# Performance work log

Measured on AMD Instinct MI355X. Metric: run time of the kernel, lower is better.

The kernel has to match this reference:

```python
import jax, jax.numpy as jnp
import numpy as np

N_NODES = 100000


def gcn_conv(x, W, b, src, dst, num_nodes):
    """PyG GCNConv: out = D^{-1/2} (A + I) D^{-1/2} (x W) + b, messages src->dst."""
    h = x @ W  # [N, out]
    # degree with self-loops (edge weight 1)
    deg = jax.ops.segment_sum(jnp.ones(src.shape[0], dtype=x.dtype), dst,
                              num_segments=num_nodes) + 1.0
    dinv = jax.lax.rsqrt(deg)  # [N]
    norm = dinv[src] * dinv[dst]  # [E]
    msg = h[src] * norm[:, None]  # gather + scale, [E, out]
    agg = jax.ops.segment_sum(msg, dst, num_segments=num_nodes)
    # self-loop term: norm_ii = dinv[i]^2
    agg = agg + h * (dinv * dinv)[:, None]
    return agg + b


def setup_inputs() -> dict:
    key = jax.random.key(0)
    ks = jax.random.split(key, 9)
    N, F_in, H1, H2, C = N_NODES, 128, 64, 32, 10
    E = 3200000
    feature = jax.random.normal(ks[0], (N, F_in), dtype=jnp.float32)
    edge_index = jax.random.randint(ks[1], (2, E), 0, N, dtype=jnp.int64)
    def glorot(k, shape):
        lim = np.sqrt(6.0 / (shape[0] + shape[1]))
        return jax.random.uniform(k, shape, jnp.float32, -lim, lim)
    return {
        "feature": feature,
        "edge_index": edge_index,
        "W1": glorot(ks[2], (F_in, H1)),
        "b1": jnp.zeros((H1,), jnp.float32),
        "W2": glorot(ks[3], (H1, H2)),
        "b2": jnp.zeros((H2,), jnp.float32),
        "Wc": glorot(ks[4], (H2, C)),
        "bc": jnp.zeros((C,), jnp.float32),
    }


def reference(feature, edge_index, W1, b1, W2, b2, Wc, bc):
    src, dst = edge_index[0], edge_index[1]
    x = gcn_conv(feature, W1, b1, src, dst, N_NODES)
    x = jax.nn.relu(x)
    # dropout is identity in eval mode
    x = gcn_conv(x, W2, b2, src, dst, N_NODES)
    x = jax.nn.relu(x)
    logits = x @ Wc + bc
    return jax.nn.log_softmax(logits, axis=1)
```

## Files before the change

kernel.cpp:

```cpp
#include <hip/hip_runtime.h>

#define N_NODES 100000
#define F_IN 128
#define H1 64
#define H2 32
#define NCLS 10

#define BS_N 256
#define NBUCK ((N_NODES + BS_N - 1) / BS_N)
#define LCAP 32
#define MCAP 9216
#define OVCAP 6144
#define STCAP 9216
#define BIN_WG 256

typedef _Float16 h2_t __attribute__((ext_vector_type(2)));

__device__ __forceinline__ float fdot2u(unsigned int u, h2_t sel, float c) {
    return __builtin_amdgcn_fdot2(__builtin_bit_cast(h2_t, u), sel, c, false);
}
__device__ __forceinline__ void accd4(float* a, uint4 v, h2_t lo, h2_t hi) {
    a[0] = fdot2u(v.x, lo, a[0]); a[1] = fdot2u(v.x, hi, a[1]);
    a[2] = fdot2u(v.y, lo, a[2]); a[3] = fdot2u(v.y, hi, a[3]);
    a[4] = fdot2u(v.z, lo, a[4]); a[5] = fdot2u(v.z, hi, a[5]);
    a[6] = fdot2u(v.w, lo, a[6]); a[7] = fdot2u(v.w, hi, a[7]);
}
__device__ __forceinline__ unsigned int pkh(float a, float b) {
    return __builtin_bit_cast(unsigned int, __builtin_amdgcn_cvt_pkrtz(a, b));
}

__global__ __launch_bounds__(512) void bin_kernel(const int* __restrict__ src,
                                                  const int* __restrict__ dst, int E,
                                                  unsigned int* __restrict__ gcur,
                                                  unsigned int* __restrict__ mainr,
                                                  unsigned int* __restrict__ ovcnt,
                                                  unsigned int* __restrict__ ovbuf) {
    __shared__ unsigned int buf[NBUCK][LCAP];
    __shared__ int cnt[NBUCK];
    int tid = threadIdx.x;
    for (int b = tid; b < NBUCK; b += 512) cnt[b] = 0;

    int chunk = (E + gridDim.x - 1) / gridDim.x;
    int e_lo = blockIdx.x * chunk;
    int e_hi = min(e_lo + chunk, E);

    int d0 = 0, s0 = 0, d1 = 0, s1 = 0;
    {
        int ea = e_lo + tid, eb = e_lo + 512 + tid;
        if (ea < e_hi) { d0 = dst[ea]; s0 = src[ea]; }
        if (eb < e_hi) { d1 = dst[eb]; s1 = src[eb]; }
    }
    __syncthreads();

    for (int base = e_lo; base < e_hi; base += 1024) {
        if (base + tid < e_hi) {
            int b = d0 >> 8;
            unsigned int en = ((unsigned int)s0 << 8) | (unsigned int)(d0 & 255);
            int p = atomicAdd(&cnt[b], 1);
            if (p < LCAP) buf[b][p] = en;
            else {
                unsigned int op = atomicAdd(&ovcnt[b * 16], 1u);
                if (op < OVCAP) ovbuf[(size_t)b * OVCAP + op] = en;
            }
        }
        if (base + 512 + tid < e_hi) {
            int b = d1 >> 8;
            unsigned int en = ((unsigned int)s1 << 8) | (unsigned int)(d1 & 255);
            int p = atomicAdd(&cnt[b], 1);
            if (p < LCAP) buf[b][p] = en;
            else {
                unsigned int op = atomicAdd(&ovcnt[b * 16], 1u);
                if (op < OVCAP) ovbuf[(size_t)b * OVCAP + op] = en;
            }
        }
        __syncthreads();
        {
            int nb = base + 1024;
            int ea = nb + tid, eb = nb + 512 + tid;
            if (ea < e_hi) { d0 = dst[ea]; s0 = src[ea]; }
            if (eb < e_hi) { d1 = dst[eb]; s1 = src[eb]; }
        }
        for (int b = tid; b < NBUCK; b += 512) {
            int c = cnt[b]; if (c > LCAP) c = LCAP;
            int nf = c & ~15;
            if (nf) {
                unsigned int gb = atomicAdd(&gcur[b * 16], (unsigned int)nf);
                if (gb + (unsigned)nf <= MCAP) {
                    for (int k = 0; k < nf; k += 4) {
                        uint4 v = make_uint4(buf[b][k], buf[b][k + 1],
                                             buf[b][k + 2], buf[b][k + 3]);
                        *(uint4*)&mainr[(size_t)b * MCAP + gb + k] = v;
                    }
                } else {
                    unsigned int op = atomicAdd(&ovcnt[b * 16], (unsigned int)nf);
                    for (int k = 0; k < nf; ++k)
                        if (op + k < OVCAP) ovbuf[(size_t)b * OVCAP + op + k] = buf[b][k];
                }
                int rem = c - nf;
                for (int k = 0; k < rem; ++k) buf[b][k] = buf[b][nf + k];
                cnt[b] = rem;
            } else {
                cnt[b] = c;
            }
        }
        __syncthreads();
    }
    for (int b = tid; b < NBUCK; b += 512) {
        int c = cnt[b]; if (c > LCAP) c = LCAP;
        if (c) {
            unsigned int ob = atomicAdd(&ovcnt[b * 16], (unsigned int)c);
            for (int k = 0; k < c; ++k)
                if (ob + k < OVCAP) ovbuf[(size_t)b * OVCAP + ob + k] = buf[b][k];
        }
    }
}

__global__ __launch_bounds__(256) void build_kernel(const unsigned int* __restrict__ gcur,
                                                    unsigned int* __restrict__ mainr,
                                                    const unsigned int* __restrict__ ovcnt,
                                                    const unsigned int* __restrict__ ovbuf,
                                                    float* __restrict__ dinv,
                                                    int2* __restrict__ row_se) {
    __shared__ unsigned int stage[STCAP];
    __shared__ int degl[BS_N];
    __shared__ int rs_l[BS_N];
    __shared__ int curl[BS_N];
    __shared__ int wtot[4];
    int b = blockIdx.x;
    int tid = threadIdx.x;

    int cm = (int)gcur[b * 16]; if (cm > MCAP) cm = MCAP;
    for (int i = tid; i < cm; i += 256) stage[i] = mainr[(size_t)b * MCAP + i];
    int co = (int)ovcnt[b * 16]; if (co > OVCAP) co = OVCAP;
    for (int i = tid; i < co; i += 256) {
        int p = cm + i;
        if (p < STCAP) stage[p] = ovbuf[(size_t)b * OVCAP + i];
    }
    int c = cm + co; if (c > STCAP) c = STCAP;
    degl[tid] = 0;
    __syncthreads();

    for (int i = tid; i < c; i += 256) atomicAdd(&degl[stage[i] & 255], 1);
    __syncthreads();

    int lane = tid & 63, w = tid >> 6;
    int d = degl[tid];
    int x = d;
    #pragma unroll
    for (int off = 1; off < 64; off <<= 1) {
        int y = __shfl_up(x, off);
        if (lane >= off) x += y;
    }
    if (lane == 63) wtot[w] = x;
    __syncthreads();
    int pbase = 0;
    #pragma unroll
    for (int k = 0; k < 4; ++k) if (k < w) pbase += wtot[k];
    rs_l[tid] = pbase + x - d;
    curl[tid] = 0;
    __syncthreads();

    size_t gbase = (size_t)b * MCAP;
    for (int i = tid; i < c; i += 256) {
        unsigned int en = stage[i];
        int dl = en & 255;
        int p = atomicAdd(&curl[dl], 1);
        mainr[gbase + rs_l[dl] + p] = en >> 8;
    }
    int node = b * BS_N + tid;
    if (node < N_NODES) {
        int deg = degl[tid];
        dinv[node] = rsqrtf((float)deg + 1.0f);
        int rs = (int)gbase + rs_l[tid];
        row_se[node] = make_int2(rs, rs + deg);
    }
}

__global__ __launch_bounds__(256) void gemm1_kernel(const float* __restrict__ X,
                                                    const float* __restrict__ W,
                                                    const float* __restrict__ dinv,
                                                    unsigned short* __restrict__ H) {
    __shared__ float Xs[64][68];
    __shared__ float Ws[F_IN * H1];
    int r0 = blockIdx.x * 64;
    const float4* W4 = (const float4*)W;
    float4* Ws4 = (float4*)Ws;
    for (int i = threadIdx.x; i < F_IN * H1 / 4; i += 256) Ws4[i] = W4[i];

    int tx = threadIdx.x & 15;
    int ty = threadIdx.x >> 4;
    float acc[4][4] = {};

    for (int kh = 0; kh < 2; ++kh) {
        __syncthreads();
        for (int it = 0; it < 4; ++it) {
            int idx = threadIdx.x + it * 256;
            int r = idx >> 4, k4 = idx & 15;
            int row = r0 + r;
            float4 v = (row < N_NODES)
                ? ((const float4*)X)[(size_t)row * 32 + kh * 16 + k4]
                : make_float4(0.f, 0.f, 0.f, 0.f);
            *(float4*)&Xs[r][k4 * 4] = v;
        }
        __syncthreads();
        #pragma unroll 8
        for (int k = 0; k < 64; ++k) {
            float4 wb = *(const float4*)&Ws[(kh * 64 + k) * H1 + tx * 4];
            float xa0 = Xs[ty * 4 + 0][k];
            float xa1 = Xs[ty * 4 + 1][k];
            float xa2 = Xs[ty * 4 + 2][k];
            float xa3 = Xs[ty * 4 + 3][k];
            acc[0][0] += xa0 * wb.x; acc[0][1] += xa0 * wb.y; acc[0][2] += xa0 * wb.z; acc[0][3] += xa0 * wb.w;
            acc[1][0] += xa1 * wb.x; acc[1][1] += xa1 * wb.y; acc[1][2] += xa1 * wb.z; acc[1][3] += xa1 * wb.w;
            acc[2][0] += xa2 * wb.x; acc[2][1] += xa2 * wb.y; acc[2][2] += xa2 * wb.z; acc[2][3] += xa2 * wb.w;
            acc[3][0] += xa3 * wb.x; acc[3][1] += xa3 * wb.y; acc[3][2] += xa3 * wb.z; acc[3][3] += xa3 * wb.w;
        }
    }
    #pragma unroll
    for (int i = 0; i < 4; ++i) {
        int row = r0 + ty * 4 + i;
        if (row < N_NODES) {
            float dv = dinv[row];
            unsigned int lo = pkh(acc[i][0] * dv, acc[i][1] * dv);
            unsigned int hi = pkh(acc[i][2] * dv, acc[i][3] * dv);
            *(uint2*)&H[(size_t)row * H1 + tx * 4] = make_uint2(lo, hi);
        }
    }
}

__global__ __launch_bounds__(256) void gemm2_kernel(const float* __restrict__ X,
                                                    const float* __restrict__ W,
                                                    const float* __restrict__ dinv,
                                                    unsigned short* __restrict__ H) {
    __shared__ float Xs[64][68];
    __shared__ float Ws[H1 * H2];
    int r0 = blockIdx.x * 64;
    const float4* W4 = (const float4*)W;
    float4* Ws4 = (float4*)Ws;
    for (int i = threadIdx.x; i < H1 * H2 / 4; i += 256) Ws4[i] = W4[i];
    for (int it = 0; it < 4; ++it) {
        int idx = threadIdx.x + it * 256;
        int r = idx >> 4, k4 = idx & 15;
        int row = r0 + r;
        float4 v = (row < N_NODES)
            ? ((const float4*)X)[(size_t)row * 16 + k4]
            : make_float4(0.f, 0.f, 0.f, 0.f);
        *(float4*)&Xs[r][k4 * 4] = v;
    }
    __syncthreads();
    int tx = threadIdx.x & 15;
    int ty = threadIdx.x >> 4;
    float acc[4][2] = {};
    #pragma unroll 8
    for (int k = 0; k < 64; ++k) {
        float2 wb = *(const float2*)&Ws[k * H2 + tx * 2];
        float xa0 = Xs[ty * 4 + 0][k];
        float xa1 = Xs[ty * 4 + 1][k];
        float xa2 = Xs[ty * 4 + 2][k];
        float xa3 = Xs[ty * 4 + 3][k];
        acc[0][0] += xa0 * wb.x; acc[0][1] += xa0 * wb.y;
        acc[1][0] += xa1 * wb.x; acc[1][1] += xa1 * wb.y;
        acc[2][0] += xa2 * wb.x; acc[2][1] += xa2 * wb.y;
        acc[3][0] += xa3 * wb.x; acc[3][1] += xa3 * wb.y;
    }
    #pragma unroll
    for (int i = 0; i < 4; ++i) {
        int row = r0 + ty * 4 + i;
        if (row < N_NODES) {
            float dv = dinv[row];
            *(unsigned int*)&H[(size_t)row * H2 + tx * 2] = pkh(acc[i][0] * dv, acc[i][1] * dv);
        }
    }
}

__global__ __launch_bounds__(256) void pull1_kernel(const unsigned short* __restrict__ h,
                                                    const unsigned int* __restrict__ csr,
                                                    const int2* __restrict__ row_se,
                                                    const float* __restrict__ dinv,
                                                    const float* __restrict__ b,
                                                    float* __restrict__ xout) {
    int wave = (blockIdx.x * 256 + threadIdx.x) >> 6;
    int lane = threadIdx.x & 63;
    int g = lane >> 3;
    int sub = lane & 7;
    int i = wave;
    int2 se = row_se[i];
    int e0 = se.x, e1 = se.y;
    int deg = e1 - e0;
    const h2_t selo = {(_Float16)1.0f, (_Float16)0.0f};
    const h2_t sehi = {(_Float16)0.0f, (_Float16)1.0f};
    float acc[8] = {};
    if (deg <= 48) {
        int sidx = (int)csr[e0 + lane];
        int i0 = __shfl(sidx, g);
        int i1 = __shfl(sidx, 8 + g);
        int i2 = __shfl(sidx, 16 + g);
        int i3 = __shfl(sidx, 24 + g);
        int i4 = __shfl(sidx, 32 + g);
        int i5 = __shfl(sidx, 40 + g);
        bool p0 = (g < deg),      p1 = (8 + g < deg),  p2 = (16 + g < deg);
        bool p3 = (24 + g < deg), p4 = (32 + g < deg), p5 = (40 + g < deg);
        uint4 v0 = make_uint4(0u, 0u, 0u, 0u), v1 = v0, v2 = v0, v3 = v0, v4 = v0, v5 = v0;
        if (p0) v0 = *(const uint4*)&h[(size_t)i0 * H1 + sub * 8];
        if (p1) v1 = *(const uint4*)&h[(size_t)i1 * H1 + sub * 8];
        if (p2) v2 = *(const uint4*)&h[(size_t)i2 * H1 + sub * 8];
        if (p3) v3 = *(const uint4*)&h[(size_t)i3 * H1 + sub * 8];
        if (p4) v4 = *(const uint4*)&h[(size_t)i4 * H1 + sub * 8];
        if (p5) v5 = *(const uint4*)&h[(size_t)i5 * H1 + sub * 8];
        if (p0) accd4(acc, v0, selo, sehi);
        if (p1) accd4(acc, v1, selo, sehi);
        if (p2) accd4(acc, v2, selo, sehi);
        if (p3) accd4(acc, v3, selo, sehi);
        if (p4) accd4(acc, v4, selo, sehi);
        if (p5) accd4(acc, v5, selo, sehi);
    } else {
        int e = e0;
        for (; e + 16 <= e1; e += 16) {
            int s0 = csr[e + g];
            int s1 = csr[e + 8 + g];
            uint4 v0 = *(const uint4*)&h[(size_t)s0 * H1 + sub * 8];
            uint4 v1 = *(const uint4*)&h[(size_t)s1 * H1 + sub * 8];
            accd4(acc, v0, selo, sehi);
            accd4(acc, v1, selo, sehi);
        }
        if (e + 8 <= e1) {
            int s = csr[e + g];
            uint4 v = *(const uint4*)&h[(size_t)s * H1 + sub * 8];
            accd4(acc, v, selo, sehi);
            e += 8;
        }
        if (e < e1) {
            int idx = e + g;
            if (idx < e1) {
                int s = csr[idx];
                uint4 v = *(const uint4*)&h[(size_t)s * H1 + sub * 8];
                accd4(acc, v, selo, sehi);
            }
        }
    }
    #pragma unroll
    for (int m = 8; m < 64; m <<= 1) {
        #pragma unroll
        for (int j = 0; j < 8; ++j) acc[j] += __shfl_xor(acc[j], m);
    }
    if (g == 0) {
        float di = dinv[i];
        uint4 sv = *(const uint4*)&h[(size_t)i * H1 + sub * 8];
        accd4(acc, sv, selo, sehi);
        float4 bb0 = *(const float4*)&b[sub * 8];
        float4 bb1 = *(const float4*)&b[sub * 8 + 4];
        float4 o0, o1;
        o0.x = fmaxf(di * acc[0] + bb0.x, 0.0f);
        o0.y = fmaxf(di * acc[1] + bb0.y, 0.0f);
        o0.z = fmaxf(di * acc[2] + bb0.z, 0.0f);
        o0.w = fmaxf(di * acc[3] + bb0.w, 0.0f);
        o1.x = fmaxf(di * acc[4] + bb1.x, 0.0f);
        o1.y = fmaxf(di * acc[5] + bb1.y, 0.0f);
        o1.z = fmaxf(di * acc[6] + bb1.z, 0.0f);
        o1.w = fmaxf(di * acc[7] + bb1.w, 0.0f);
        *(float4*)&xout[(size_t)i * H1 + sub * 8] = o0;
        *(float4*)&xout[(size_t)i * H1 + sub * 8 + 4] = o1;
    }
}

__global__ __launch_bounds__(256) void pull2_kernel(const unsigned short* __restrict__ h,
                                                    const unsigned int* __restrict__ csr,
                                                    const int2* __restrict__ row_se,
                                                    const float* __restrict__ dinv,
                                                    const float* __restrict__ b,
                                                    float* __restrict__ xout) {
    int wave = (blockIdx.x * 256 + threadIdx.x) >> 6;
    int lane = threadIdx.x & 63;
    int g = lane >> 2;
    int sub = lane & 3;
    int i = wave;
    int2 se = row_se[i];
    int e0 = se.x, e1 = se.y;
    int deg = e1 - e0;
    const h2_t selo = {(_Float16)1.0f, (_Float16)0.0f};
    const h2_t sehi = {(_Float16)0.0f, (_Float16)1.0f};
    float acc[8] = {};
    if (deg <= 48) {
        int sidx = (int)csr[e0 + lane];
        int i0 = __shfl(sidx, g);
        int i1 = __shfl(sidx, 16 + g);
        int i2 = __shfl(sidx, 32 + g);
        bool p0 = (g < deg), p1 = (16 + g < deg), p2 = (32 + g < deg);
        uint4 v0 = make_uint4(0u, 0u, 0u, 0u), v1 = v0, v2 = v0;
        if (p0) v0 = *(const uint4*)&h[(size_t)i0 * H2 + sub * 8];
        if (p1) v1 = *(const uint4*)&h[(size_t)i1 * H2 + sub * 8];
        if (p2) v2 = *(const uint4*)&h[(size_t)i2 * H2 + sub * 8];
        if (p0) accd4(acc, v0, selo, sehi);
        if (p1) accd4(acc, v1, selo, sehi);
        if (p2) accd4(acc, v2, selo, sehi);
    } else {
        int e = e0;
        for (; e + 32 <= e1; e += 32) {
            int s0 = csr[e + g];
            int s1 = csr[e + 16 + g];
            uint4 v0 = *(const uint4*)&h[(size_t)s0 * H2 + sub * 8];
            uint4 v1 = *(const uint4*)&h[(size_t)s1 * H2 + sub * 8];
            accd4(acc, v0, selo, sehi);
            accd4(acc, v1, selo, sehi);
        }
        if (e + 16 <= e1) {
            int s = csr[e + g];
            uint4 v = *(const uint4*)&h[(size_t)s * H2 + sub * 8];
            accd4(acc, v, selo, sehi);
            e += 16;
        }
        if (e < e1) {
            int idx = e + g;
            if (idx < e1) {
                int s = csr[idx];
                uint4 v = *(const uint4*)&h[(size_t)s * H2 + sub * 8];
                accd4(acc, v, selo, sehi);
            }
        }
    }
    #pragma unroll
    for (int m = 4; m < 64; m <<= 1) {
        #pragma unroll
        for (int j = 0; j < 8; ++j) acc[j] += __shfl_xor(acc[j], m);
    }
    if (g == 0) {
        float di = dinv[i];
        uint4 sv = *(const uint4*)&h[(size_t)i * H2 + sub * 8];
        accd4(acc, sv, selo, sehi);
        float4 bb0 = *(const float4*)&b[sub * 8];
        float4 bb1 = *(const float4*)&b[sub * 8 + 4];
        float4 o0, o1;
        o0.x = fmaxf(di * acc[0] + bb0.x, 0.0f);
        o0.y = fmaxf(di * acc[1] + bb0.y, 0.0f);
        o0.z = fmaxf(di * acc[2] + bb0.z, 0.0f);
        o0.w = fmaxf(di * acc[3] + bb0.w, 0.0f);
        o1.x = fmaxf(di * acc[4] + bb1.x, 0.0f);
        o1.y = fmaxf(di * acc[5] + bb1.y, 0.0f);
        o1.z = fmaxf(di * acc[6] + bb1.z, 0.0f);
        o1.w = fmaxf(di * acc[7] + bb1.w, 0.0f);
        *(float4*)&xout[(size_t)i * H2 + sub * 8] = o0;
        *(float4*)&xout[(size_t)i * H2 + sub * 8 + 4] = o1;
    }
}

__global__ __launch_bounds__(256) void final_kernel(const float* __restrict__ X2,
                                                    const float* __restrict__ Wc,
                                                    const float* __restrict__ bc,
                                                    float* __restrict__ out) {
    __shared__ float Ws[H2 * NCLS];
    __shared__ float bs[NCLS];
    for (int idx = threadIdx.x; idx < H2 * NCLS; idx += 256) Ws[idx] = Wc[idx];
    if (threadIdx.x < NCLS) bs[threadIdx.x] = bc[threadIdx.x];
    __syncthreads();
    int i = blockIdx.x * blockDim.x + threadIdx.x;
    if (i >= N_NODES) return;
    float x[H2];
    #pragma unroll
    for (int k = 0; k < H2; ++k) x[k] = X2[(size_t)i * H2 + k];
    float lg[NCLS];
    #pragma unroll
    for (int c = 0; c < NCLS; ++c) {
        float acc = bs[c];
        #pragma unroll
        for (int k = 0; k < H2; ++k) acc += x[k] * Ws[k * NCLS + c];
        lg[c] = acc;
    }
    float m = lg[0];
    #pragma unroll
    for (int c = 1; c < NCLS; ++c) m = fmaxf(m, lg[c]);
    float s = 0.0f;
    #pragma unroll
    for (int c = 0; c < NCLS; ++c) s += expf(lg[c] - m);
    float lse = m + logf(s);
    #pragma unroll
    for (int c = 0; c < NCLS; ++c) out[(size_t)i * NCLS + c] = lg[c] - lse;
}

extern "C" void kernel_launch(void* const* d_in, const int* in_sizes, int n_in,
                              void* d_out, int out_size, void* d_ws, size_t ws_size,
                              hipStream_t stream) {
    const float* feature = (const float*)d_in[0];
    const int*   eidx    = (const int*)d_in[1];
    const float* W1      = (const float*)d_in[2];
    const float* b1      = (const float*)d_in[3];
    const float* W2      = (const float*)d_in[4];
    const float* b2      = (const float*)d_in[5];
    const float* Wc      = (const float*)d_in[6];
    const float* bc      = (const float*)d_in[7];
    float* out = (float*)d_out;

    const int E = in_sizes[1] / 2;
    const int* src = eidx;
    const int* dst = eidx + E;

    float*          ws        = (float*)d_ws;
    float*          dinv      = ws;
    int2*           row_se    = (int2*)(dinv + N_NODES);
    unsigned int*   gcur      = (unsigned int*)(row_se + N_NODES);
    unsigned int*   ovcnt     = gcur + (size_t)NBUCK * 16;
    unsigned int*   ovbuf     = ovcnt + (size_t)NBUCK * 16;
    unsigned int*   mainr     = ovbuf + (size_t)NBUCK * OVCAP;
    unsigned short* h1b       = (unsigned short*)(mainr + (size_t)NBUCK * MCAP);
    float*          x1        = (float*)(h1b + (size_t)N_NODES * H1);
    unsigned short* h2b       = h1b;
    float*          x2        = x1;

    hipMemsetAsync(gcur, 0, (size_t)NBUCK * 32 * sizeof(unsigned int), stream);
    bin_kernel<<<BIN_WG, 512, 0, stream>>>(src, dst, E, gcur, mainr, ovcnt, ovbuf);
    build_kernel<<<NBUCK, 256, 0, stream>>>(gcur, mainr, ovcnt, ovbuf, dinv, row_se);

    gemm1_kernel<<<(N_NODES + 63) / 64, 256, 0, stream>>>(feature, W1, dinv, h1b);
    {
        unsigned int grid = (unsigned int)(((size_t)N_NODES * 64 + 255) / 256);
        pull1_kernel<<<grid, 256, 0, stream>>>(h1b, mainr, row_se, dinv, b1, x1);
    }

    gemm2_kernel<<<(N_NODES + 63) / 64, 256, 0, stream>>>(x1, W2, dinv, h2b);
    {
        unsigned int grid = (unsigned int)(((size_t)N_NODES * 64 + 255) / 256);
        pull2_kernel<<<grid, 256, 0, stream>>>(h2b, mainr, row_se, dinv, b2, x2);
    }

    final_kernel<<<(N_NODES + 255) / 256, 256, 0, stream>>>(x2, Wc, bc, out);
}
```

Before: 302.5 us.

## Use MFMA fp16 for first GEMM and fuse classifier into second pull

The first feature transform is rewritten to convert X and W1 to fp16 in shared memory and compute with 16x16x32 MFMA instructions, staging the output through shared memory for coalesced stores. Separately, the final linear layer plus log-softmax is fused into the second aggregation kernel using cross-lane shuffles, removing a kernel launch and the write/read of the intermediate x2. The MFMA path lowers input precision of X and W1 to fp16, and the fused epilogue adds shared-memory setup to every pull2 block.

```diff
diff --git a/kernel.cpp b/kernel.cpp
--- a/kernel.cpp
+++ b/kernel.cpp
@@ -15,6 +15,8 @@
 #define BIN_WG 256
 
 typedef _Float16 h2_t __attribute__((ext_vector_type(2)));
+typedef _Float16 f16x8 __attribute__((ext_vector_type(8)));
+typedef float f32x4 __attribute__((ext_vector_type(4)));
 
 __device__ __forceinline__ float fdot2u(unsigned int u, h2_t sel, float c) {
     return __builtin_amdgcn_fdot2(__builtin_bit_cast(h2_t, u), sel, c, false);
@@ -180,51 +182,60 @@
                                                     const float* __restrict__ W,
                                                     const float* __restrict__ dinv,
                                                     unsigned short* __restrict__ H) {
-    __shared__ float Xs[64][68];
-    __shared__ float Ws[F_IN * H1];
+    __shared__ union {
+        struct {
+            _Float16 As[64][136];
+            _Float16 Wf[16][64][8];
+        } s;
+        _Float16 Hs[64][72];
+    } u;
     int r0 = blockIdx.x * 64;
-    const float4* W4 = (const float4*)W;
-    float4* Ws4 = (float4*)Ws;
-    for (int i = threadIdx.x; i < F_IN * H1 / 4; i += 256) Ws4[i] = W4[i];
-
-    int tx = threadIdx.x & 15;
-    int ty = threadIdx.x >> 4;
-    float acc[4][4] = {};
-
-    for (int kh = 0; kh < 2; ++kh) {
-        __syncthreads();
-        for (int it = 0; it < 4; ++it) {
-            int idx = threadIdx.x + it * 256;
-            int r = idx >> 4, k4 = idx & 15;
-            int row = r0 + r;
-            float4 v = (row < N_NODES)
-                ? ((const float4*)X)[(size_t)row * 32 + kh * 16 + k4]
-                : make_float4(0.f, 0.f, 0.f, 0.f);
-            *(float4*)&Xs[r][k4 * 4] = v;
-        }
-        __syncthreads();
-        #pragma unroll 8
-        for (int k = 0; k < 64; ++k) {
-            float4 wb = *(const float4*)&Ws[(kh * 64 + k) * H1 + tx * 4];
-            float xa0 = Xs[ty * 4 + 0][k];
-            float xa1 = Xs[ty * 4 + 1][k];
-            float xa2 = Xs[ty * 4 + 2][k];
-            float xa3 = Xs[ty * 4 + 3][k];
-            acc[0][0] += xa0 * wb.x; acc[0][1] += xa0 * wb.y; acc[0][2] += xa0 * wb.z; acc[0][3] += xa0 * wb.w;
-            acc[1][0] += xa1 * wb.x; acc[1][1] += xa1 * wb.y; acc[1][2] += xa1 * wb.z; acc[1][3] += xa1 * wb.w;
-            acc[2][0] += xa2 * wb.x; acc[2][1] += xa2 * wb.y; acc[2][2] += xa2 * wb.z; acc[2][3] += xa2 * wb.w;
-            acc[3][0] += xa3 * wb.x; acc[3][1] += xa3 * wb.y; acc[3][2] += xa3 * wb.z; acc[3][3] += xa3 * wb.w;
-        }
-    }
-    #pragma unroll
-    for (int i = 0; i < 4; ++i) {
-        int row = r0 + ty * 4 + i;
-        if (row < N_NODES) {
-            float dv = dinv[row];
-            unsigned int lo = pkh(acc[i][0] * dv, acc[i][1] * dv);
-            unsigned int hi = pkh(acc[i][2] * dv, acc[i][3] * dv);
-            *(uint2*)&H[(size_t)row * H1 + tx * 4] = make_uint2(lo, hi);
-        }
+    int tid = threadIdx.x;
+    for (int i = tid; i < 2048; i += 256) {
+        int row = i >> 5, k4 = i & 31;
+        int grow = r0 + row;
+        float4 v = (grow < N_NODES) ? ((const float4*)X)[(size_t)grow * 32 + k4]
+                                    : make_float4(0.f, 0.f, 0.f, 0.f);
+        _Float16 t4[4] = {(_Float16)v.x, (_Float16)v.y, (_Float16)v.z, (_Float16)v.w};
+        *(uint2*)&u.s.As[row][k4 * 4] = *(uint2*)t4;
+    }
+    for (int i = tid; i < F_IN * H1; i += 256) {
+        int k = i >> 6, col = i & 63;
+        u.s.Wf[k >> 3][col][k & 7] = (_Float16)W[i];
+    }
+    __syncthreads();
+
+    int lane = tid & 63, w = tid >> 6;
+    int lr = lane & 15, lkg = lane >> 4;
+    f32x4 acc[4] = {{0.f, 0.f, 0.f, 0.f}, {0.f, 0.f, 0.f, 0.f},
+                    {0.f, 0.f, 0.f, 0.f}, {0.f, 0.f, 0.f, 0.f}};
+    #pragma unroll
+    for (int ks = 0; ks < 4; ++ks) {
+        f16x8 a = *(const f16x8*)&u.s.As[w * 16 + lr][ks * 32 + lkg * 8];
+        #pragma unroll
+        for (int nt = 0; nt < 4; ++nt) {
+            f16x8 bfr = *(const f16x8*)&u.s.Wf[ks * 4 + lkg][nt * 16 + lr][0];
+            acc[nt] = __builtin_amdgcn_mfma_f32_16x16x32_f16(a, bfr, acc[nt], 0, 0, 0);
+        }
+    }
+    __syncthreads();
+    float dv[4];
+    #pragma unroll
+    for (int q = 0; q < 4; ++q) {
+        int grow = r0 + w * 16 + lkg * 4 + q;
+        dv[q] = (grow < N_NODES) ? dinv[grow] : 0.f;
+    }
+    #pragma unroll
+    for (int nt = 0; nt < 4; ++nt)
+        #pragma unroll
+        for (int q = 0; q < 4; ++q)
+            u.Hs[w * 16 + lkg * 4 + q][nt * 16 + lr] = (_Float16)(acc[nt][q] * dv[q]);
+    __syncthreads();
+    for (int i = tid; i < 512; i += 256) {
+        int row = i >> 3, seg = i & 7;
+        int grow = r0 + row;
+        if (grow < N_NODES)
+            *(uint4*)&H[(size_t)grow * H1 + seg * 8] = *(const uint4*)&u.Hs[row][seg * 8];
     }
 }
 
@@ -368,7 +379,15 @@
                                                     const int2* __restrict__ row_se,
                                                     const float* __restrict__ dinv,
                                                     const float* __restrict__ b,
-                                                    float* __restrict__ xout) {
+                                                    const float* __restrict__ Wc,
+                                                    const float* __restrict__ bc,
+                                                    float* __restrict__ out) {
+    __shared__ float WsL[H2 * NCLS];
+    __shared__ float bsL[NCLS];
+    for (int idx = threadIdx.x; idx < H2 * NCLS; idx += 256) WsL[idx] = Wc[idx];
+    if (threadIdx.x < NCLS) bsL[threadIdx.x] = bc[threadIdx.x];
+    __syncthreads();
+
     int wave = (blockIdx.x * 256 + threadIdx.x) >> 6;
     int lane = threadIdx.x & 63;
     int g = lane >> 2;
@@ -429,51 +448,44 @@
         accd4(acc, sv, selo, sehi);
         float4 bb0 = *(const float4*)&b[sub * 8];
         float4 bb1 = *(const float4*)&b[sub * 8 + 4];
-        float4 o0, o1;
-        o0.x = fmaxf(di * acc[0] + bb0.x, 0.0f);
-        o0.y = fmaxf(di * acc[1] + bb0.y, 0.0f);
-        o0.z = fmaxf(di * acc[2] + bb0.z, 0.0f);
-        o0.w = fmaxf(di * acc[3] + bb0.w, 0.0f);
-        o1.x = fmaxf(di * acc[4] + bb1.x, 0.0f);
-        o1.y = fmaxf(di * acc[5] + bb1.y, 0.0f);
-        o1.z = fmaxf(di * acc[6] + bb1.z, 0.0f);
-        o1.w = fmaxf(di * acc[7] + bb1.w, 0.0f);
-        *(float4*)&xout[(size_t)i * H2 + sub * 8] = o0;
-        *(float4*)&xout[(size_t)i * H2 + sub * 8 + 4] = o1;
-    }
-}
-
-__global__ __launch_bounds__(256) void final_kernel(const float* __restrict__ X2,
-                                                    const float* __restrict__ Wc,
-                                                    const float* __restrict__ bc,
-                                                    float* __restrict__ out) {
-    __shared__ float Ws[H2 * NCLS];
-    __shared__ float bs[NCLS];
-    for (int idx = threadIdx.x; idx < H2 * NCLS; idx += 256) Ws[idx] = Wc[idx];
-    if (threadIdx.x < NCLS) bs[threadIdx.x] = bc[threadIdx.x];
-    __syncthreads();
-    int i = blockIdx.x * blockDim.x + threadIdx.x;
-    if (i >= N_NODES) return;
-    float x[H2];
-    #pragma unroll
-    for (int k = 0; k < H2; ++k) x[k] = X2[(size_t)i * H2 + k];
-    float lg[NCLS];
-    #pragma unroll
-    for (int c = 0; c < NCLS; ++c) {
-        float acc = bs[c];
-        #pragma unroll
-        for (int k = 0; k < H2; ++k) acc += x[k] * Ws[k * NCLS + c];
-        lg[c] = acc;
-    }
-    float m = lg[0];
-    #pragma unroll
-    for (int c = 1; c < NCLS; ++c) m = fmaxf(m, lg[c]);
-    float s = 0.0f;
-    #pragma unroll
-    for (int c = 0; c < NCLS; ++c) s += expf(lg[c] - m);
-    float lse = m + logf(s);
-    #pragma unroll
-    for (int c = 0; c < NCLS; ++c) out[(size_t)i * NCLS + c] = lg[c] - lse;
+        float x[8];
+        x[0] = fmaxf(di * acc[0] + bb0.x, 0.0f);
+        x[1] = fmaxf(di * acc[1] + bb0.y, 0.0f);
+        x[2] = fmaxf(di * acc[2] + bb0.z, 0.0f);
+        x[3] = fmaxf(di * acc[3] + bb0.w, 0.0f);
+        x[4] = fmaxf(di * acc[4] + bb1.x, 0.0f);
+        x[5] = fmaxf(di * acc[5] + bb1.y, 0.0f);
+        x[6] = fmaxf(di * acc[6] + bb1.z, 0.0f);
+        x[7] = fmaxf(di * acc[7] + bb1.w, 0.0f);
+        float lgt[NCLS];
+        #pragma unroll
+        for (int c2 = 0; c2 < NCLS; ++c2) {
+            float a2 = 0.f;
+            #pragma unroll
+            for (int j = 0; j < 8; ++j) a2 += x[j] * WsL[(sub * 8 + j) * NCLS + c2];
+            lgt[c2] = a2;
+        }
+        #pragma unroll
+        for (int c2 = 0; c2 < NCLS; ++c2) lgt[c2] += __shfl_xor(lgt[c2], 1);
+        #pragma unroll
+        for (int c2 = 0; c2 < NCLS; ++c2) lgt[c2] += __shfl_xor(lgt[c2], 2);
+        if (sub == 0) {
+            float m2 = -1e30f;
+            #pragma unroll
+            for (int c2 = 0; c2 < NCLS; ++c2) {
+                lgt[c2] += bsL[c2];
+                m2 = fmaxf(m2, lgt[c2]);
+            }
+            float s2 = 0.f;
+            #pragma unroll
+            for (int c2 = 0; c2 < NCLS; ++c2) s2 += expf(lgt[c2] - m2);
+            float lse = m2 + logf(s2);
+            float* op = &out[(size_t)i * NCLS];
+            #pragma unroll
+            for (int c2 = 0; c2 < NCLS; c2 += 2)
+                *(float2*)&op[c2] = make_float2(lgt[c2] - lse, lgt[c2 + 1] - lse);
+        }
+    }
 }
 
 extern "C" void kernel_launch(void* const* d_in, const int* in_sizes, int n_in,
@@ -503,7 +515,6 @@
     unsigned short* h1b       = (unsigned short*)(mainr + (size_t)NBUCK * MCAP);
     float*          x1        = (float*)(h1b + (size_t)N_NODES * H1);
     unsigned short* h2b       = h1b;
-    float*          x2        = x1;
 
     hipMemsetAsync(gcur, 0, (size_t)NBUCK * 32 * sizeof(unsigned int), stream);
     bin_kernel<<<BIN_WG, 512, 0, stream>>>(src, dst, E, gcur, mainr, ovcnt, ovbuf);
@@ -518,8 +529,6 @@
     gemm2_kernel<<<(N_NODES + 63) / 64, 256, 0, stream>>>(x1, W2, dinv, h2b);
     {
         unsigned int grid = (unsigned int)(((size_t)N_NODES * 64 + 255) / 256);
-        pull2_kernel<<<grid, 256, 0, stream>>>(h2b, mainr, row_se, dinv, b2, x2);
-    }
-
-    final_kernel<<<(N_NODES + 255) / 256, 256, 0, stream>>>(x2, Wc, bc, out);
-}
+        pull2_kernel<<<grid, 256, 0, stream>>>(h2b, mainr, row_se, dinv, b2, Wc, bc, out);
+    }
+}
```

Result: slower. 319.3 us (+5.5%).
